# Performance work log

Hardware: AMD Instinct MI355X
Metric: run time of the kernel (lower is better)

Reference implementation:

```python
import jax, jax.numpy as jnp
import numpy as np

B, T, S = 16, 128, 128          # batch, temporal, spatial (road segments)
NIN, SIN = 3, 1                 # number / speed input feature sizes
NH, SH, DH = 64, 64, 128        # number-enc / speed-enc / decoder hidden
T_PREDICT = 20


def _p(k, shape, scale=0.05):
    return (jax.random.normal(k, shape) * scale).astype(jnp.float32)


def setup_inputs() -> dict:
    key = jax.random.key(0)
    ks = jax.random.split(key, 16)
    inp = {"input_data": jax.random.normal(ks[0], (B, T, S, NIN + SIN), dtype=jnp.float32)}
    # seg_model cells: LSTM gates driven by input x, own hidden h, spatial neighbors h_after/h_before
    inp.update(
        n_Wx=_p(ks[1], (NIN, 4 * NH)), n_Wh=_p(ks[2], (NH, 4 * NH)),
        n_Wa=_p(ks[3], (NH, 4 * NH)), n_Wb=_p(ks[4], (NH, 4 * NH)),
        n_b=jnp.zeros((4 * NH,), jnp.float32),
        s_Wx=_p(ks[5], (SIN, 4 * SH)), s_Wh=_p(ks[6], (SH, 4 * SH)),
        s_Wa=_p(ks[7], (SH, 4 * SH)), s_Wb=_p(ks[8], (SH, 4 * SH)),
        s_b=jnp.zeros((4 * SH,), jnp.float32),
        d_Wx=_p(ks[9], (NH + SH, 4 * DH)), d_Wh=_p(ks[10], (DH, 4 * DH)),
        d_Wa=_p(ks[11], (DH, 4 * DH)), d_Wb=_p(ks[12], (DH, 4 * DH)),
        d_b=jnp.zeros((4 * DH,), jnp.float32),
        on_W=_p(ks[13], (DH, 1)), on_b=jnp.zeros((1,), jnp.float32),
        os_W=_p(ks[14], (DH, 1)), os_b=jnp.zeros((1,), jnp.float32),
    )
    return inp


def _cell(x, h, c, ha, hb, Wx, Wh, Wa, Wb, b):
    g = x @ Wx + h @ Wh + ha @ Wa + hb @ Wb + b
    i, f, u, o = jnp.split(g, 4, axis=-1)
    c2 = jax.nn.sigmoid(f) * c + jax.nn.sigmoid(i) * jnp.tanh(u)
    return jax.nn.sigmoid(o) * jnp.tanh(c2), c2


def _shift(h):
    # h_after[s] = h[s+1], h_before[s] = h[s-1], zero-padded at the boundary
    z = jnp.zeros_like(h[:, :1])
    return jnp.concatenate([h[:, 1:], z], axis=1), jnp.concatenate([z, h[:, :-1]], axis=1)


def _next_input(former_number, next_x, output):
    # output: [B,S,2] = (number_out, speed_out)
    speed_in = next_x[:, :1, 3:]                                    # [B,1,1]
    speed_next = jnp.concatenate([speed_in, output[:, 1:, 1:]], axis=1)
    inflow = jnp.concatenate([next_x[:, 0:1, 1:2], output[:, :-1, 0:1]], axis=1)
    number_calc = former_number[:, :, 2:3] + inflow - output[:, :, 0:1]
    return jnp.concatenate([output[:, :, 0:1], inflow, number_calc, speed_next], axis=2)


def reference(input_data, n_Wx, n_Wh, n_Wa, n_Wb, n_b,
              s_Wx, s_Wh, s_Wa, s_Wb, s_b,
              d_Wx, d_Wh, d_Wa, d_Wb, d_b,
              on_W, on_b, os_W, os_b):
    b, t, s, _ = input_data.shape
    zeros = lambda hdim: jnp.zeros((b, s, hdim), input_data.dtype)
    init = (zeros(NH), zeros(NH), zeros(SH), zeros(SH), zeros(DH), zeros(DH))

    def step(carry, xs):
        hn, cn, hs, cs, hd, cd = carry
        x_t, x_tp1 = xs
        hn_a, hn_b = _shift(hn)
        hs_a, hs_b = _shift(hs)
        hd_a, hd_b = _shift(hd)
        num = x_t[:, :, :NIN]
        spd = x_t[:, :, NIN:]
        hn, cn = _cell(num, hn, cn, hn_a, hn_b, n_Wx, n_Wh, n_Wa, n_Wb, n_b)
        hs, cs = _cell(spd, hs, cs, hs_a, hs_b, s_Wx, s_Wh, s_Wa, s_Wb, s_b)
        dec_in = jnp.concatenate([hn, hs], axis=2)
        hd, cd = _cell(dec_in, hd, cd, hd_a, hd_b, d_Wx, d_Wh, d_Wa, d_Wb, d_b)
        output = jnp.concatenate([hd @ on_W + on_b, hd @ os_W + os_b], axis=2)
        data = _next_input(num, x_tp1, output)
        return (hn, cn, hs, cs, hd, cd), data

    xs = (jnp.moveaxis(input_data[:, :-1], 1, 0),   # x_t,   t = 0..T-2 (time-major)
          jnp.moveaxis(input_data[:, 1:], 1, 0))    # x_{t+1}
    _, datas = jax.lax.scan(step, init, xs)          # [T-1, B, S, 4]
    # original writes outputs only for time >= t_predict; slicing is equivalent
    return jnp.moveaxis(datas[T_PREDICT:], 0, 1)     # [B, T-T_PREDICT-1, S, 4]
```

## Files before the change

kernel.cpp:

```cpp
#include <hip/hip_runtime.h>

constexpr int B_ = 16, T_ = 128, S_ = 128;
constexpr int ROWS = B_ * S_;
constexpr int NSTEPS = T_ - 1;
constexpr int TPRED = 20;
constexpr int TOUT = NSTEPS - TPRED;
constexpr int RPB = 16;
constexpr int TB = 512;
constexpr int NBLK = 256;

constexpr int OFF_HN = 0;
constexpr int OFF_HS = OFF_HN + 131072;
constexpr int OFF_HD = OFF_HS + 131072;
constexpr int OFF_CN = OFF_HD + 262144;
constexpr int OFF_CS = OFF_CN + 131072;
constexpr int OFF_CD = OFF_CS + 131072;
constexpr int OFF_GP = OFF_CD + 262144;
constexpr int OFF_OUTS = OFF_GP + 2097152;
constexpr int ZERO_DW = OFF_GP;
constexpr int OFF_NPK = OFF_OUTS + NSTEPS * ROWS * 2;
constexpr int NPK_DW = 16 * 7 * 256;
constexpr int OFF_SPK = OFF_NPK + NPK_DW;
constexpr int OFF_DPK = OFF_SPK + NPK_DW;
constexpr int DPK_DW = 32 * 16 * 256;
constexpr int PACK_DWORDS = 2 * NPK_DW + DPK_DW;

typedef _Float16 half8 __attribute__((ext_vector_type(8)));
typedef float float4v __attribute__((ext_vector_type(4)));

__device__ __forceinline__ float sigm(float x) { return 1.f / (1.f + __expf(-x)); }
__device__ __forceinline__ float tanh_(float x) { return 2.f / (1.f + __expf(-2.f * x)) - 1.f; }
__device__ __forceinline__ unsigned int pack2(float a, float b) {
    union { unsigned int u; _Float16 h[2]; } x;
    x.h[0] = (_Float16)a; x.h[1] = (_Float16)b; return x.u;
}

__global__ __launch_bounds__(256) void pack_weights(
    const float* __restrict__ nWx, const float* __restrict__ nWh,
    const float* __restrict__ nWa, const float* __restrict__ nWb, const float* __restrict__ nb,
    const float* __restrict__ sWx, const float* __restrict__ sWh,
    const float* __restrict__ sWa, const float* __restrict__ sWb, const float* __restrict__ sb,
    const float* __restrict__ dWx, const float* __restrict__ dWh,
    const float* __restrict__ dWa, const float* __restrict__ dWb,
    unsigned int* __restrict__ wsu)
{
    int idx = blockIdx.x * 256 + threadIdx.x;
    if (idx >= PACK_DWORDS) return;
    if (idx < 2 * NPK_DW) {
        bool isS = idx >= NPK_DW;
        int dn = isS ? idx - NPK_DW : idx;
        int tile = dn >> 8;
        int e = (dn & 255) * 2;
        int lane = e >> 3, j0 = e & 7;
        int quad = lane >> 4;
        int nt = tile / 7, tt = tile % 7;
        int col = nt * 16 + (lane & 15);
        float v0, v1;
        if (tt < 6) {
            const float* W = isS ? ((tt < 2) ? sWh : (tt < 4) ? sWa : sWb)
                                 : ((tt < 2) ? nWh : (tt < 4) ? nWa : nWb);
            int k = (tt & 1) * 32 + quad * 8 + j0;
            v0 = W[k * 256 + col]; v1 = W[(k + 1) * 256 + col];
        } else {
            int kl = quad * 8 + j0;
            auto xv = [&](int k) -> float {
                if (!isS) { if (k < 3) return nWx[k * 256 + col]; if (k == 3) return nb[col]; return 0.f; }
                else      { if (k == 4) return sWx[col]; if (k == 5) return sb[col]; return 0.f; }
            };
            v0 = xv(kl); v1 = xv(kl + 1);
        }
        wsu[(isS ? OFF_SPK : OFF_NPK) + dn] = pack2(v0, v1);
    } else {
        int dd = idx - 2 * NPK_DW;
        int tile = dd >> 8;
        int e = (dd & 255) * 2;
        int lane = e >> 3, j0 = e & 7;
        int quad = lane >> 4;
        int nt = tile >> 4, tt = tile & 15;
        const float* W = (tt < 4) ? dWx : (tt < 8) ? dWh : (tt < 12) ? dWa : dWb;
        int k = (tt & 3) * 32 + quad * 8 + j0;
        int col = nt * 16 + (lane & 15);
        wsu[OFF_DPK + dd] = pack2(W[k * 512 + col], W[(k + 1) * 512 + col]);
    }
}

__global__ __launch_bounds__(TB) void pipe_kernel(
    int li,
    const float* __restrict__ input,
    const float* __restrict__ db,
    const float* __restrict__ onW, const float* __restrict__ onb,
    const float* __restrict__ osW, const float* __restrict__ osb,
    float* __restrict__ ws)
{
    const int tid = threadIdx.x;
    const int wave = tid >> 6, lane = tid & 63;
    const int quad = lane >> 4, l15 = lane & 15;
    const int blk = blockIdx.x;

    _Float16* hnG = (_Float16*)((unsigned int*)ws + OFF_HN);
    _Float16* hsG = (_Float16*)((unsigned int*)ws + OFF_HS);
    _Float16* hdG = (_Float16*)((unsigned int*)ws + OFF_HD);
    float* cn = ws + OFF_CN;
    float* cs = ws + OFF_CS;
    float* cd = ws + OFF_CD;
    float* gpart = ws + OFF_GP;
    float* outs = ws + OFF_OUTS;
    const _Float16* pd = (const _Float16*)((const unsigned int*)ws + OFF_DPK);

    __shared__ __align__(16) _Float16 sh_hn[18 * 72];
    __shared__ __align__(16) _Float16 sh_hs[18 * 72];
    __shared__ __align__(16) _Float16 sh_xa[16 * 40];
    __shared__ __align__(16) _Float16 sh_dec[16 * 136];
    __shared__ __align__(16) _Float16 sh_hd[18 * 136];
    __shared__ float sh_hdnew[16 * 128];

    if (blk < 128) {
        if (li > 126) return;
        const int ab = blk;
        const int r0 = ab * RPB;
        const int b = r0 >> 7;
        const int s0 = r0 & 127;
        const bool leftOK = (ab & 7) != 0;
        const bool rightOK = (ab & 7) != 7;
        const int pin = (li + 1) & 1, pout = li & 1;
        const _Float16* hnC = hnG + (size_t)pin * ROWS * 64;
        const _Float16* hsC = hsG + (size_t)pin * ROWS * 64;
        _Float16* hnN = hnG + (size_t)pout * ROWS * 64;
        _Float16* hsN = hsG + (size_t)pout * ROWS * 64;

        for (int i = tid; i < 1152; i += TB) {
            bool isHs = i >= 576;
            int j = isHs ? i - 576 : i;
            int row = j >> 5, p = j & 31;
            int grow = r0 + row - 1;
            bool v = (row == 0) ? leftOK : ((row == 17) ? rightOK : true);
            const _Float16* src = isHs ? hsC : hnC;
            unsigned int val = v ? ((const unsigned int*)src)[(size_t)grow * 32 + p] : 0u;
            _Float16* dst = isHs ? sh_hs : sh_hn;
            *(unsigned int*)(dst + row * 72 + 2 * p) = val;
        }
        for (int i = tid; i < 272; i += TB) {
            int r = i / 17, d = 3 + (i % 17);
            ((unsigned int*)sh_xa)[r * 20 + d] = 0u;
        }
        if (tid < 16) {
            const float* xp = input + ((size_t)(b * T_ + li) * S_ + (s0 + tid)) * 4;
            unsigned int* row = (unsigned int*)sh_xa + tid * 20;
            row[0] = pack2(xp[0], xp[1]);
            row[1] = pack2(xp[2], 1.f);
            row[2] = pack2(xp[3], 1.f);
        }
        __syncthreads();

        {
            const int subA = wave & 3;
            const bool isS = (wave >= 4);
            const _Float16* hb = isS ? sh_hs : sh_hn;
            const _Float16* pk = (const _Float16*)((const unsigned int*)ws + (isS ? OFF_SPK : OFF_NPK));
            half8 ah0 = *(const half8*)(hb + (l15 + 1) * 72 + quad * 8);
            half8 ah1 = *(const half8*)(hb + (l15 + 1) * 72 + 32 + quad * 8);
            half8 aa0 = *(const half8*)(hb + (l15 + 2) * 72 + quad * 8);
            half8 aa1 = *(const half8*)(hb + (l15 + 2) * 72 + 32 + quad * 8);
            half8 ab0 = *(const half8*)(hb + (l15) * 72 + quad * 8);
            half8 ab1 = *(const half8*)(hb + (l15) * 72 + 32 + quad * 8);
            half8 ax  = *(const half8*)(sh_xa + l15 * 40 + quad * 8);
            float4v acc[4];
#pragma unroll
            for (int g = 0; g < 4; ++g) acc[g] = (float4v){0.f, 0.f, 0.f, 0.f};
#pragma unroll
            for (int g = 0; g < 4; ++g) {
                const _Float16* base = pk + (size_t)(4 * g + subA) * 7 * 512 + lane * 8;
                acc[g] = __builtin_amdgcn_mfma_f32_16x16x32_f16(ah0, *(const half8*)(base),        acc[g], 0, 0, 0);
                acc[g] = __builtin_amdgcn_mfma_f32_16x16x32_f16(ah1, *(const half8*)(base + 512),  acc[g], 0, 0, 0);
                acc[g] = __builtin_amdgcn_mfma_f32_16x16x32_f16(aa0, *(const half8*)(base + 1024), acc[g], 0, 0, 0);
                acc[g] = __builtin_amdgcn_mfma_f32_16x16x32_f16(aa1, *(const half8*)(base + 1536), acc[g], 0, 0, 0);
                acc[g] = __builtin_amdgcn_mfma_f32_16x16x32_f16(ab0, *(const half8*)(base + 2048), acc[g], 0, 0, 0);
                acc[g] = __builtin_amdgcn_mfma_f32_16x16x32_f16(ab1, *(const half8*)(base + 2560), acc[g], 0, 0, 0);
                acc[g] = __builtin_amdgcn_mfma_f32_16x16x32_f16(ax,  *(const half8*)(base + 3072), acc[g], 0, 0, 0);
            }
            float* cB = isS ? cs : cn;
            size_t cIdx = ((size_t)(ab * 4 + subA) * 64 + lane) * 4;
            float4v cold = *(const float4v*)(cB + cIdx);
            float4v cnew;
            _Float16* hN = isS ? hsN : hnN;
            const int kcol = 16 * subA + l15;
#pragma unroll
            for (int r = 0; r < 4; ++r) {
                float c2 = sigm(acc[1][r]) * cold[r] + sigm(acc[0][r]) * tanh_(acc[2][r]);
                float h2 = sigm(acc[3][r]) * tanh_(c2);
                cnew[r] = c2;
                int row = quad * 4 + r;
                hN[(size_t)(r0 + row) * 64 + kcol] = (_Float16)h2;
                sh_dec[row * 136 + (isS ? 64 : 0) + kcol] = (_Float16)h2;
            }
            *(float4v*)(cB + cIdx) = cnew;
        }
        __syncthreads();

        {
            const int ct = wave;
            half8 aD[4];
#pragma unroll
            for (int kt = 0; kt < 4; ++kt)
                aD[kt] = *(const half8*)(sh_dec + l15 * 136 + kt * 32 + quad * 8);
            float4v accP[4];
#pragma unroll
            for (int g = 0; g < 4; ++g) accP[g] = (float4v){0.f, 0.f, 0.f, 0.f};
#pragma unroll
            for (int g = 0; g < 4; ++g) {
                const _Float16* base = pd + (size_t)(g * 8 + ct) * 16 * 512 + lane * 8;
#pragma unroll
                for (int kt = 0; kt < 4; ++kt)
                    accP[g] = __builtin_amdgcn_mfma_f32_16x16x32_f16(aD[kt], *(const half8*)(base + kt * 512), accP[g], 0, 0, 0);
            }
            float* gp = gpart + ((((size_t)(li & 1) * 128 + ab) * 8 + ct) * 4) * 256;
#pragma unroll
            for (int g = 0; g < 4; ++g)
                *(float4v*)&gp[g * 256 + lane * 4] = accP[g];
        }
    } else {
        if (li < 1) return;
        const int bb = blk - 128;
        const int t = li - 1;
        const int r0 = bb * RPB;
        const bool leftOK = (bb & 7) != 0;
        const bool rightOK = (bb & 7) != 7;
        const int pinD = li & 1;
        const int poutD = (li + 1) & 1;
        const _Float16* hdC = hdG + (size_t)pinD * ROWS * 128;
        _Float16* hdN = hdG + (size_t)poutD * ROWS * 128;

        for (int i = tid; i < 1152; i += TB) {
            int row = i >> 6, p = i & 63;
            int grow = r0 + row - 1;
            bool v = (row == 0) ? leftOK : ((row == 17) ? rightOK : true);
            unsigned int val = v ? ((const unsigned int*)hdC)[(size_t)grow * 64 + p] : 0u;
            *(unsigned int*)(sh_hd + row * 136 + 2 * p) = val;
        }
        __syncthreads();

        {
            const int ct = wave;
            const float* gp = gpart + ((((size_t)((li + 1) & 1) * 128 + bb) * 8 + ct) * 4) * 256;
            float4v acc[4];
#pragma unroll
            for (int g = 0; g < 4; ++g) acc[g] = *(const float4v*)&gp[g * 256 + lane * 4];
            half8 aH[4], aA[4], aB4[4];
#pragma unroll
            for (int kt = 0; kt < 4; ++kt) {
                aH[kt]  = *(const half8*)(sh_hd + (l15 + 1) * 136 + kt * 32 + quad * 8);
                aA[kt]  = *(const half8*)(sh_hd + (l15 + 2) * 136 + kt * 32 + quad * 8);
                aB4[kt] = *(const half8*)(sh_hd + (l15) * 136 + kt * 32 + quad * 8);
            }
#pragma unroll
            for (int g = 0; g < 4; ++g) {
                const _Float16* base = pd + (size_t)(g * 8 + ct) * 16 * 512 + lane * 8;
#pragma unroll
                for (int kt = 0; kt < 4; ++kt)
                    acc[g] = __builtin_amdgcn_mfma_f32_16x16x32_f16(aH[kt], *(const half8*)(base + (4 + kt) * 512), acc[g], 0, 0, 0);
#pragma unroll
                for (int kt = 0; kt < 4; ++kt)
                    acc[g] = __builtin_amdgcn_mfma_f32_16x16x32_f16(aA[kt], *(const half8*)(base + (8 + kt) * 512), acc[g], 0, 0, 0);
#pragma unroll
                for (int kt = 0; kt < 4; ++kt)
                    acc[g] = __builtin_amdgcn_mfma_f32_16x16x32_f16(aB4[kt], *(const half8*)(base + (12 + kt) * 512), acc[g], 0, 0, 0);
            }
            const int kd = 16 * ct + l15;
            float bi = db[kd], bf = db[128 + kd], bu = db[256 + kd], bo = db[384 + kd];
            float* cPtr = cd + ((size_t)(bb * 8 + ct) * 64 + lane) * 4;
            float4v cold = *(float4v*)cPtr, cnew;
#pragma unroll
            for (int r = 0; r < 4; ++r) {
                float c2 = sigm(acc[1][r] + bf) * cold[r] + sigm(acc[0][r] + bi) * tanh_(acc[2][r] + bu);
                float h2 = sigm(acc[3][r] + bo) * tanh_(c2);
                cnew[r] = c2;
                int row = quad * 4 + r;
                hdN[(size_t)(r0 + row) * 128 + kd] = (_Float16)h2;
                sh_hdnew[row * 128 + kd] = h2;
            }
            *(float4v*)cPtr = cnew;
        }
        __syncthreads();

        {
            int p = tid >> 4, l16 = tid & 15;
            int row = p >> 1, head = p & 1;
            const float* W = head ? osW : onW;
            float partial = 0.f;
#pragma unroll
            for (int k = 0; k < 128; k += 16) partial += sh_hdnew[row * 128 + k + l16] * W[k + l16];
#pragma unroll
            for (int off = 8; off; off >>= 1) partial += __shfl_down(partial, off, 16);
            if (l16 == 0)
                outs[((size_t)t * ROWS + (r0 + row)) * 2 + head] = partial + (head ? osb[0] : onb[0]);
        }
    }
}

__global__ __launch_bounds__(256) void assemble_kernel(
    const float* __restrict__ input, const float* __restrict__ ws, float* __restrict__ out)
{
    const float* outs = ws + OFF_OUTS;
    int idx = blockIdx.x * 256 + threadIdx.x;
    if (idx >= B_ * TOUT * S_) return;
    int s = idx & 127;
    int tmp = idx >> 7;
    int tt = tmp % TOUT;
    int b = tmp / TOUT;
    int t = tt + TPRED;
    int row = b * S_ + s;
    float o0 = outs[((size_t)t * ROWS + row) * 2 + 0];
    float o1 = outs[((size_t)t * ROWS + row) * 2 + 1];
    float inflow = (s == 0) ? input[(((size_t)b * T_ + (t + 1)) * S_ + 0) * 4 + 1]
                            : outs[((size_t)t * ROWS + row - 1) * 2 + 0];
    float numc = input[(((size_t)b * T_ + t) * S_ + s) * 4 + 2] + inflow - o0;
    float spd = (s == 0) ? input[(((size_t)b * T_ + (t + 1)) * S_ + 0) * 4 + 3] : o1;
    float4 v = make_float4(o0, inflow, numc, spd);
    reinterpret_cast<float4*>(out)[idx] = v;
}

extern "C" void kernel_launch(void* const* d_in, const int* in_sizes, int n_in,
                              void* d_out, int out_size, void* d_ws, size_t ws_size,
                              hipStream_t stream) {
    const float* input = (const float*)d_in[0];
    const float* nWx = (const float*)d_in[1];
    const float* nWh = (const float*)d_in[2];
    const float* nWa = (const float*)d_in[3];
    const float* nWb = (const float*)d_in[4];
    const float* nb  = (const float*)d_in[5];
    const float* sWx = (const float*)d_in[6];
    const float* sWh = (const float*)d_in[7];
    const float* sWa = (const float*)d_in[8];
    const float* sWb = (const float*)d_in[9];
    const float* sb  = (const float*)d_in[10];
    const float* dWx = (const float*)d_in[11];
    const float* dWh = (const float*)d_in[12];
    const float* dWa = (const float*)d_in[13];
    const float* dWb = (const float*)d_in[14];
    const float* db  = (const float*)d_in[15];
    const float* onW = (const float*)d_in[16];
    const float* onb = (const float*)d_in[17];
    const float* osW = (const float*)d_in[18];
    const float* osb = (const float*)d_in[19];

    float* ws = (float*)d_ws;

    hipMemsetAsync(ws, 0, (size_t)ZERO_DW * 4, stream);

    pack_weights<<<dim3((PACK_DWORDS + 255) / 256), dim3(256), 0, stream>>>(
        nWx, nWh, nWa, nWb, nb, sWx, sWh, sWa, sWb, sb,
        dWx, dWh, dWa, dWb, (unsigned int*)ws);

    for (int li = 0; li <= NSTEPS; ++li) {
        pipe_kernel<<<dim3(NBLK), dim3(TB), 0, stream>>>(
            li, input, db, onW, onb, osW, osb, ws);
    }

    int nout = B_ * TOUT * S_;
    assemble_kernel<<<dim3((nout + 255) / 256), dim3(256), 0, stream>>>(input, ws, (float*)d_out);
}
```

Measured before the change: 1.232 ms.

## Repartition pipeline blocks: split encoder by cell, decoder by column half, drop gate-partial buffer

```diff
diff --git a/kernel.cpp b/kernel.cpp
--- a/kernel.cpp
+++ b/kernel.cpp
@@ -5,7 +5,6 @@
 constexpr int NSTEPS = T_ - 1;
 constexpr int TPRED = 20;
 constexpr int TOUT = NSTEPS - TPRED;
-constexpr int RPB = 16;
 constexpr int TB = 512;
 constexpr int NBLK = 256;
 
@@ -15,10 +14,9 @@
 constexpr int OFF_CN = OFF_HD + 262144;
 constexpr int OFF_CS = OFF_CN + 131072;
 constexpr int OFF_CD = OFF_CS + 131072;
-constexpr int OFF_GP = OFF_CD + 262144;
-constexpr int OFF_OUTS = OFF_GP + 2097152;
-constexpr int ZERO_DW = OFF_GP;
-constexpr int OFF_NPK = OFF_OUTS + NSTEPS * ROWS * 2;
+constexpr int OFF_OUTS = OFF_CD + 262144;
+constexpr int ZERO_DW = OFF_OUTS + NSTEPS * ROWS * 2;
+constexpr int OFF_NPK = ZERO_DW;
 constexpr int NPK_DW = 16 * 7 * 256;
 constexpr int OFF_SPK = OFF_NPK + NPK_DW;
 constexpr int OFF_DPK = OFF_SPK + NPK_DW;
@@ -88,8 +86,7 @@
     int li,
     const float* __restrict__ input,
     const float* __restrict__ db,
-    const float* __restrict__ onW, const float* __restrict__ onb,
-    const float* __restrict__ osW, const float* __restrict__ osb,
+    const float* __restrict__ onW, const float* __restrict__ osW,
     float* __restrict__ ws)
 {
     const int tid = threadIdx.x;
@@ -100,50 +97,40 @@
     _Float16* hnG = (_Float16*)((unsigned int*)ws + OFF_HN);
     _Float16* hsG = (_Float16*)((unsigned int*)ws + OFF_HS);
     _Float16* hdG = (_Float16*)((unsigned int*)ws + OFF_HD);
-    float* cn = ws + OFF_CN;
-    float* cs = ws + OFF_CS;
-    float* cd = ws + OFF_CD;
-    float* gpart = ws + OFF_GP;
     float* outs = ws + OFF_OUTS;
     const _Float16* pd = (const _Float16*)((const unsigned int*)ws + OFF_DPK);
 
-    __shared__ __align__(16) _Float16 sh_hn[18 * 72];
-    __shared__ __align__(16) _Float16 sh_hs[18 * 72];
-    __shared__ __align__(16) _Float16 sh_xa[16 * 40];
-    __shared__ __align__(16) _Float16 sh_dec[16 * 136];
-    __shared__ __align__(16) _Float16 sh_hd[18 * 136];
-    __shared__ float sh_hdnew[16 * 128];
+    __shared__ __align__(16) _Float16 sh_h[34 * 72];
+    __shared__ __align__(16) _Float16 sh_xa[32 * 40];
+    __shared__ __align__(16) _Float16 sh_hd[34 * 136];
+    __shared__ __align__(16) _Float16 sh_dec[32 * 136];
+    __shared__ float sh_hdnew[32 * 64];
 
     if (blk < 128) {
         if (li > 126) return;
-        const int ab = blk;
-        const int r0 = ab * RPB;
+        const int pr = blk >> 1, cell = blk & 1;
+        const int r0 = pr * 32;
         const int b = r0 >> 7;
         const int s0 = r0 & 127;
-        const bool leftOK = (ab & 7) != 0;
-        const bool rightOK = (ab & 7) != 7;
+        const bool leftOK = (pr & 3) != 0;
+        const bool rightOK = (pr & 3) != 3;
         const int pin = (li + 1) & 1, pout = li & 1;
-        const _Float16* hnC = hnG + (size_t)pin * ROWS * 64;
-        const _Float16* hsC = hsG + (size_t)pin * ROWS * 64;
-        _Float16* hnN = hnG + (size_t)pout * ROWS * 64;
-        _Float16* hsN = hsG + (size_t)pout * ROWS * 64;
-
-        for (int i = tid; i < 1152; i += TB) {
-            bool isHs = i >= 576;
-            int j = isHs ? i - 576 : i;
-            int row = j >> 5, p = j & 31;
+        const _Float16* hC = (cell ? hsG : hnG) + (size_t)pin * ROWS * 64;
+        _Float16* hN = (cell ? hsG : hnG) + (size_t)pout * ROWS * 64;
+        float* cB = ws + (cell ? OFF_CS : OFF_CN);
+
+        for (int i = tid; i < 1088; i += TB) {
+            int row = i >> 5, p = i & 31;
             int grow = r0 + row - 1;
-            bool v = (row == 0) ? leftOK : ((row == 17) ? rightOK : true);
-            const _Float16* src = isHs ? hsC : hnC;
-            unsigned int val = v ? ((const unsigned int*)src)[(size_t)grow * 32 + p] : 0u;
-            _Float16* dst = isHs ? sh_hs : sh_hn;
-            *(unsigned int*)(dst + row * 72 + 2 * p) = val;
-        }
-        for (int i = tid; i < 272; i += TB) {
+            bool v = (row == 0) ? leftOK : ((row == 33) ? rightOK : true);
+            unsigned int val = v ? ((const unsigned int*)hC)[(size_t)grow * 32 + p] : 0u;
+            *(unsigned int*)(sh_h + row * 72 + 2 * p) = val;
+        }
+        for (int i = tid; i < 544; i += TB) {
             int r = i / 17, d = 3 + (i % 17);
             ((unsigned int*)sh_xa)[r * 20 + d] = 0u;
         }
-        if (tid < 16) {
+        if (tid < 32) {
             const float* xp = input + ((size_t)(b * T_ + li) * S_ + (s0 + tid)) * 4;
             unsigned int* row = (unsigned int*)sh_xa + tid * 20;
             row[0] = pack2(xp[0], xp[1]);
@@ -152,153 +139,140 @@
         }
         __syncthreads();
 
-        {
-            const int subA = wave & 3;
-            const bool isS = (wave >= 4);
-            const _Float16* hb = isS ? sh_hs : sh_hn;
-            const _Float16* pk = (const _Float16*)((const unsigned int*)ws + (isS ? OFF_SPK : OFF_NPK));
-            half8 ah0 = *(const half8*)(hb + (l15 + 1) * 72 + quad * 8);
-            half8 ah1 = *(const half8*)(hb + (l15 + 1) * 72 + 32 + quad * 8);
-            half8 aa0 = *(const half8*)(hb + (l15 + 2) * 72 + quad * 8);
-            half8 aa1 = *(const half8*)(hb + (l15 + 2) * 72 + 32 + quad * 8);
-            half8 ab0 = *(const half8*)(hb + (l15) * 72 + quad * 8);
-            half8 ab1 = *(const half8*)(hb + (l15) * 72 + 32 + quad * 8);
-            half8 ax  = *(const half8*)(sh_xa + l15 * 40 + quad * 8);
-            float4v acc[4];
-#pragma unroll
-            for (int g = 0; g < 4; ++g) acc[g] = (float4v){0.f, 0.f, 0.f, 0.f};
-#pragma unroll
-            for (int g = 0; g < 4; ++g) {
-                const _Float16* base = pk + (size_t)(4 * g + subA) * 7 * 512 + lane * 8;
-                acc[g] = __builtin_amdgcn_mfma_f32_16x16x32_f16(ah0, *(const half8*)(base),        acc[g], 0, 0, 0);
-                acc[g] = __builtin_amdgcn_mfma_f32_16x16x32_f16(ah1, *(const half8*)(base + 512),  acc[g], 0, 0, 0);
-                acc[g] = __builtin_amdgcn_mfma_f32_16x16x32_f16(aa0, *(const half8*)(base + 1024), acc[g], 0, 0, 0);
-                acc[g] = __builtin_amdgcn_mfma_f32_16x16x32_f16(aa1, *(const half8*)(base + 1536), acc[g], 0, 0, 0);
-                acc[g] = __builtin_amdgcn_mfma_f32_16x16x32_f16(ab0, *(const half8*)(base + 2048), acc[g], 0, 0, 0);
-                acc[g] = __builtin_amdgcn_mfma_f32_16x16x32_f16(ab1, *(const half8*)(base + 2560), acc[g], 0, 0, 0);
-                acc[g] = __builtin_amdgcn_mfma_f32_16x16x32_f16(ax,  *(const half8*)(base + 3072), acc[g], 0, 0, 0);
-            }
-            float* cB = isS ? cs : cn;
-            size_t cIdx = ((size_t)(ab * 4 + subA) * 64 + lane) * 4;
-            float4v cold = *(const float4v*)(cB + cIdx);
-            float4v cnew;
-            _Float16* hN = isS ? hsN : hnN;
-            const int kcol = 16 * subA + l15;
-#pragma unroll
-            for (int r = 0; r < 4; ++r) {
-                float c2 = sigm(acc[1][r]) * cold[r] + sigm(acc[0][r]) * tanh_(acc[2][r]);
-                float h2 = sigm(acc[3][r]) * tanh_(c2);
-                cnew[r] = c2;
-                int row = quad * 4 + r;
-                hN[(size_t)(r0 + row) * 64 + kcol] = (_Float16)h2;
-                sh_dec[row * 136 + (isS ? 64 : 0) + kcol] = (_Float16)h2;
-            }
-            *(float4v*)(cB + cIdx) = cnew;
-        }
-        __syncthreads();
-
-        {
-            const int ct = wave;
-            half8 aD[4];
-#pragma unroll
-            for (int kt = 0; kt < 4; ++kt)
-                aD[kt] = *(const half8*)(sh_dec + l15 * 136 + kt * 32 + quad * 8);
-            float4v accP[4];
-#pragma unroll
-            for (int g = 0; g < 4; ++g) accP[g] = (float4v){0.f, 0.f, 0.f, 0.f};
-#pragma unroll
-            for (int g = 0; g < 4; ++g) {
-                const _Float16* base = pd + (size_t)(g * 8 + ct) * 16 * 512 + lane * 8;
-#pragma unroll
-                for (int kt = 0; kt < 4; ++kt)
-                    accP[g] = __builtin_amdgcn_mfma_f32_16x16x32_f16(aD[kt], *(const half8*)(base + kt * 512), accP[g], 0, 0, 0);
-            }
-            float* gp = gpart + ((((size_t)(li & 1) * 128 + ab) * 8 + ct) * 4) * 256;
-#pragma unroll
-            for (int g = 0; g < 4; ++g)
-                *(float4v*)&gp[g * 256 + lane * 4] = accP[g];
-        }
+        const int tl = wave >> 2, sub = wave & 3;
+        const _Float16* pk = (const _Float16*)((const unsigned int*)ws + (cell ? OFF_SPK : OFF_NPK));
+        const int rb = 1 + tl * 16 + l15;
+        half8 ah0 = *(const half8*)(sh_h + rb * 72 + quad * 8);
+        half8 ah1 = *(const half8*)(sh_h + rb * 72 + 32 + quad * 8);
+        half8 aa0 = *(const half8*)(sh_h + (rb + 1) * 72 + quad * 8);
+        half8 aa1 = *(const half8*)(sh_h + (rb + 1) * 72 + 32 + quad * 8);
+        half8 ab0 = *(const half8*)(sh_h + (rb - 1) * 72 + quad * 8);
+        half8 ab1 = *(const half8*)(sh_h + (rb - 1) * 72 + 32 + quad * 8);
+        half8 ax  = *(const half8*)(sh_xa + (tl * 16 + l15) * 40 + quad * 8);
+        float4v acc[4];
+#pragma unroll
+        for (int g = 0; g < 4; ++g) acc[g] = (float4v){0.f, 0.f, 0.f, 0.f};
+#pragma unroll
+        for (int g = 0; g < 4; ++g) {
+            const _Float16* base = pk + (size_t)(4 * g + sub) * 7 * 512 + lane * 8;
+            acc[g] = __builtin_amdgcn_mfma_f32_16x16x32_f16(ah0, *(const half8*)(base),        acc[g], 0, 0, 0);
+            acc[g] = __builtin_amdgcn_mfma_f32_16x16x32_f16(ah1, *(const half8*)(base + 512),  acc[g], 0, 0, 0);
+            acc[g] = __builtin_amdgcn_mfma_f32_16x16x32_f16(aa0, *(const half8*)(base + 1024), acc[g], 0, 0, 0);
+            acc[g] = __builtin_amdgcn_mfma_f32_16x16x32_f16(aa1, *(const half8*)(base + 1536), acc[g], 0, 0, 0);
+            acc[g] = __builtin_amdgcn_mfma_f32_16x16x32_f16(ab0, *(const half8*)(base + 2048), acc[g], 0, 0, 0);
+            acc[g] = __builtin_amdgcn_mfma_f32_16x16x32_f16(ab1, *(const half8*)(base + 2560), acc[g], 0, 0, 0);
+            acc[g] = __builtin_amdgcn_mfma_f32_16x16x32_f16(ax,  *(const half8*)(base + 3072), acc[g], 0, 0, 0);
+        }
+        size_t cIdx = ((size_t)((pr * 2 + tl) * 4 + sub) * 64 + lane) * 4;
+        float4v cold = *(const float4v*)(cB + cIdx);
+        float4v cnew;
+        const int kcol = 16 * sub + l15;
+#pragma unroll
+        for (int r = 0; r < 4; ++r) {
+            float c2 = sigm(acc[1][r]) * cold[r] + sigm(acc[0][r]) * tanh_(acc[2][r]);
+            float h2 = sigm(acc[3][r]) * tanh_(c2);
+            cnew[r] = c2;
+            int row = tl * 16 + quad * 4 + r;
+            hN[(size_t)(r0 + row) * 64 + kcol] = (_Float16)h2;
+        }
+        *(float4v*)(cB + cIdx) = cnew;
     } else {
         if (li < 1) return;
         const int bb = blk - 128;
+        const int pr = bb >> 1, ch = bb & 1;
         const int t = li - 1;
-        const int r0 = bb * RPB;
-        const bool leftOK = (bb & 7) != 0;
-        const bool rightOK = (bb & 7) != 7;
+        const int r0 = pr * 32;
+        const bool leftOK = (pr & 3) != 0;
+        const bool rightOK = (pr & 3) != 3;
         const int pinD = li & 1;
-        const int poutD = (li + 1) & 1;
+        const int poutD = (li - 1) & 1;
+        const int pdec = (li - 1) & 1;
         const _Float16* hdC = hdG + (size_t)pinD * ROWS * 128;
         _Float16* hdN = hdG + (size_t)poutD * ROWS * 128;
-
-        for (int i = tid; i < 1152; i += TB) {
+        const _Float16* hnC = hnG + (size_t)pdec * ROWS * 64;
+        const _Float16* hsC = hsG + (size_t)pdec * ROWS * 64;
+        float* cd = ws + OFF_CD;
+
+        for (int i = tid; i < 2176; i += TB) {
             int row = i >> 6, p = i & 63;
             int grow = r0 + row - 1;
-            bool v = (row == 0) ? leftOK : ((row == 17) ? rightOK : true);
+            bool v = (row == 0) ? leftOK : ((row == 33) ? rightOK : true);
             unsigned int val = v ? ((const unsigned int*)hdC)[(size_t)grow * 64 + p] : 0u;
             *(unsigned int*)(sh_hd + row * 136 + 2 * p) = val;
         }
+        for (int i = tid; i < 2048; i += TB) {
+            bool isHs = i >= 1024;
+            int j = isHs ? i - 1024 : i;
+            int r = j >> 5, p = j & 31;
+            const unsigned int* src = (const unsigned int*)(isHs ? hsC : hnC);
+            *(unsigned int*)(sh_dec + r * 136 + (isHs ? 64 : 0) + 2 * p) = src[(size_t)(r0 + r) * 32 + p];
+        }
         __syncthreads();
 
+        const int tl = wave >> 2, sub = wave & 3;
+        const int rb = 1 + tl * 16 + l15;
+        const int rdec = tl * 16 + l15;
+        half8 aD[4], aH[4], aA[4], aB4[4];
+#pragma unroll
+        for (int kt = 0; kt < 4; ++kt) {
+            aD[kt]  = *(const half8*)(sh_dec + rdec * 136 + kt * 32 + quad * 8);
+            aH[kt]  = *(const half8*)(sh_hd + rb * 136 + kt * 32 + quad * 8);
+            aA[kt]  = *(const half8*)(sh_hd + (rb + 1) * 136 + kt * 32 + quad * 8);
+            aB4[kt] = *(const half8*)(sh_hd + (rb - 1) * 136 + kt * 32 + quad * 8);
+        }
+        float4v acc[4];
+#pragma unroll
+        for (int g = 0; g < 4; ++g) acc[g] = (float4v){0.f, 0.f, 0.f, 0.f};
+#pragma unroll
+        for (int g = 0; g < 4; ++g) {
+            const _Float16* base = pd + (size_t)(g * 8 + ch * 4 + sub) * 16 * 512 + lane * 8;
+#pragma unroll
+            for (int kt = 0; kt < 4; ++kt)
+                acc[g] = __builtin_amdgcn_mfma_f32_16x16x32_f16(aD[kt],  *(const half8*)(base + kt * 512),        acc[g], 0, 0, 0);
+#pragma unroll
+            for (int kt = 0; kt < 4; ++kt)
+                acc[g] = __builtin_amdgcn_mfma_f32_16x16x32_f16(aH[kt],  *(const half8*)(base + (4 + kt) * 512),  acc[g], 0, 0, 0);
+#pragma unroll
+            for (int kt = 0; kt < 4; ++kt)
+                acc[g] = __builtin_amdgcn_mfma_f32_16x16x32_f16(aA[kt],  *(const half8*)(base + (8 + kt) * 512),  acc[g], 0, 0, 0);
+#pragma unroll
+            for (int kt = 0; kt < 4; ++kt)
+                acc[g] = __builtin_amdgcn_mfma_f32_16x16x32_f16(aB4[kt], *(const half8*)(base + (12 + kt) * 512), acc[g], 0, 0, 0);
+        }
+        const int kd = ch * 64 + sub * 16 + l15;
+        float bi = db[kd], bf = db[128 + kd], bu = db[256 + kd], bo = db[384 + kd];
+        float* cPtr = cd + ((size_t)(((pr * 2 + ch) * 2 + tl) * 4 + sub) * 64 + lane) * 4;
+        float4v cold = *(float4v*)cPtr, cnew;
+#pragma unroll
+        for (int r = 0; r < 4; ++r) {
+            float c2 = sigm(acc[1][r] + bf) * cold[r] + sigm(acc[0][r] + bi) * tanh_(acc[2][r] + bu);
+            float h2 = sigm(acc[3][r] + bo) * tanh_(c2);
+            cnew[r] = c2;
+            int row = tl * 16 + quad * 4 + r;
+            hdN[(size_t)(r0 + row) * 128 + kd] = (_Float16)h2;
+            sh_hdnew[row * 64 + sub * 16 + l15] = h2;
+        }
+        *(float4v*)cPtr = cnew;
+        __syncthreads();
+
         {
-            const int ct = wave;
-            const float* gp = gpart + ((((size_t)((li + 1) & 1) * 128 + bb) * 8 + ct) * 4) * 256;
-            float4v acc[4];
-#pragma unroll
-            for (int g = 0; g < 4; ++g) acc[g] = *(const float4v*)&gp[g * 256 + lane * 4];
-            half8 aH[4], aA[4], aB4[4];
-#pragma unroll
-            for (int kt = 0; kt < 4; ++kt) {
-                aH[kt]  = *(const half8*)(sh_hd + (l15 + 1) * 136 + kt * 32 + quad * 8);
-                aA[kt]  = *(const half8*)(sh_hd + (l15 + 2) * 136 + kt * 32 + quad * 8);
-                aB4[kt] = *(const half8*)(sh_hd + (l15) * 136 + kt * 32 + quad * 8);
-            }
-#pragma unroll
-            for (int g = 0; g < 4; ++g) {
-                const _Float16* base = pd + (size_t)(g * 8 + ct) * 16 * 512 + lane * 8;
-#pragma unroll
-                for (int kt = 0; kt < 4; ++kt)
-                    acc[g] = __builtin_amdgcn_mfma_f32_16x16x32_f16(aH[kt], *(const half8*)(base + (4 + kt) * 512), acc[g], 0, 0, 0);
-#pragma unroll
-                for (int kt = 0; kt < 4; ++kt)
-                    acc[g] = __builtin_amdgcn_mfma_f32_16x16x32_f16(aA[kt], *(const half8*)(base + (8 + kt) * 512), acc[g], 0, 0, 0);
-#pragma unroll
-                for (int kt = 0; kt < 4; ++kt)
-                    acc[g] = __builtin_amdgcn_mfma_f32_16x16x32_f16(aB4[kt], *(const half8*)(base + (12 + kt) * 512), acc[g], 0, 0, 0);
-            }
-            const int kd = 16 * ct + l15;
-            float bi = db[kd], bf = db[128 + kd], bu = db[256 + kd], bo = db[384 + kd];
-            float* cPtr = cd + ((size_t)(bb * 8 + ct) * 64 + lane) * 4;
-            float4v cold = *(float4v*)cPtr, cnew;
-#pragma unroll
-            for (int r = 0; r < 4; ++r) {
-                float c2 = sigm(acc[1][r] + bf) * cold[r] + sigm(acc[0][r] + bi) * tanh_(acc[2][r] + bu);
-                float h2 = sigm(acc[3][r] + bo) * tanh_(c2);
-                cnew[r] = c2;
-                int row = quad * 4 + r;
-                hdN[(size_t)(r0 + row) * 128 + kd] = (_Float16)h2;
-                sh_hdnew[row * 128 + kd] = h2;
-            }
-            *(float4v*)cPtr = cnew;
-        }
-        __syncthreads();
-
-        {
-            int p = tid >> 4, l16 = tid & 15;
+            int p = tid >> 3, l8 = tid & 7;
             int row = p >> 1, head = p & 1;
-            const float* W = head ? osW : onW;
+            const float* W = (head ? osW : onW) + ch * 64;
             float partial = 0.f;
 #pragma unroll
-            for (int k = 0; k < 128; k += 16) partial += sh_hdnew[row * 128 + k + l16] * W[k + l16];
-#pragma unroll
-            for (int off = 8; off; off >>= 1) partial += __shfl_down(partial, off, 16);
-            if (l16 == 0)
-                outs[((size_t)t * ROWS + (r0 + row)) * 2 + head] = partial + (head ? osb[0] : onb[0]);
+            for (int k = 0; k < 64; k += 8) partial += sh_hdnew[row * 64 + k + l8] * W[k + l8];
+#pragma unroll
+            for (int off = 4; off; off >>= 1) partial += __shfl_down(partial, off, 8);
+            if (l8 == 0) atomicAdd(&outs[((size_t)t * ROWS + (r0 + row)) * 2 + head], partial);
         }
     }
 }
 
 __global__ __launch_bounds__(256) void assemble_kernel(
-    const float* __restrict__ input, const float* __restrict__ ws, float* __restrict__ out)
+    const float* __restrict__ input, const float* __restrict__ ws,
+    const float* __restrict__ onb, const float* __restrict__ osb,
+    float* __restrict__ out)
 {
     const float* outs = ws + OFF_OUTS;
     int idx = blockIdx.x * 256 + threadIdx.x;
@@ -309,10 +283,11 @@
     int b = tmp / TOUT;
     int t = tt + TPRED;
     int row = b * S_ + s;
-    float o0 = outs[((size_t)t * ROWS + row) * 2 + 0];
-    float o1 = outs[((size_t)t * ROWS + row) * 2 + 1];
+    float ob0 = onb[0], ob1 = osb[0];
+    float o0 = outs[((size_t)t * ROWS + row) * 2 + 0] + ob0;
+    float o1 = outs[((size_t)t * ROWS + row) * 2 + 1] + ob1;
     float inflow = (s == 0) ? input[(((size_t)b * T_ + (t + 1)) * S_ + 0) * 4 + 1]
-                            : outs[((size_t)t * ROWS + row - 1) * 2 + 0];
+                            : (outs[((size_t)t * ROWS + row - 1) * 2 + 0] + ob0);
     float numc = input[(((size_t)b * T_ + t) * S_ + s) * 4 + 2] + inflow - o0;
     float spd = (s == 0) ? input[(((size_t)b * T_ + (t + 1)) * S_ + 0) * 4 + 3] : o1;
     float4 v = make_float4(o0, inflow, numc, spd);
@@ -353,9 +328,10 @@
 
     for (int li = 0; li <= NSTEPS; ++li) {
         pipe_kernel<<<dim3(NBLK), dim3(TB), 0, stream>>>(
-            li, input, db, onW, onb, osW, osb, ws);
+            li, input, db, onW, osW, ws);
     }
 
     int nout = B_ * TOUT * S_;
-    assemble_kernel<<<dim3((nout + 255) / 256), dim3(256), 0, stream>>>(input, ws, (float*)d_out);
-}
+    assemble_kernel<<<dim3((nout + 255) / 256), dim3(256), 0, stream>>>(
+        input, ws, onb, osb, (float*)d_out);
+}
```

Result: slower. 1.410 ms (+14.4%).
